# Kernel tuning notes

Measured on AMD Instinct MI355X. Metric: run time of the kernel, lower is better.

## Reference

```python
import jax, jax.numpy as jnp
import numpy as np

B, S, D, H = 4, 1024, 1024, 16
DH = D // H  # 64
SCALE = 1.0 / np.sqrt(D)  # module uses 1/sqrt(d_model), not d_head


def _mh(t):
    # [B,S,D] -> [B*H,S,DH]
    b, s, _ = t.shape
    return t.reshape(b, s, H, DH).transpose(0, 2, 1, 3).reshape(b * H, s, DH)


def _shift(t):
    # pad one zero at FRONT of last dim, reinterpret (row-major) as [BH,L+1,S], drop first row
    bh, s, l = t.shape
    t = jnp.concatenate([jnp.zeros((bh, s, 1), t.dtype), t], axis=-1)
    return t.reshape(bh, l + 1, s)[:, 1:, :]


def setup_inputs() -> dict:
    key = jax.random.key(0)
    ks = jax.random.split(key, 12)
    w_sc = 1.0 / np.sqrt(D)
    return {
        "x": jax.random.normal(ks[0], (B, S, D), jnp.float32),
        "u": jax.random.normal(ks[1], (DH,), jnp.float32) * 0.02,
        "v": jax.random.normal(ks[2], (DH,), jnp.float32) * 0.02,
        "pos": jax.random.normal(ks[3], (B, S, D), jnp.float32),
        "Wq": jax.random.normal(ks[4], (D, D), jnp.float32) * w_sc,
        "bq": jnp.zeros((D,), jnp.float32),
        "Wk": jax.random.normal(ks[5], (D, D), jnp.float32) * w_sc,
        "bk": jnp.zeros((D,), jnp.float32),
        "Wv": jax.random.normal(ks[6], (D, D), jnp.float32) * w_sc,
        "bv": jnp.zeros((D,), jnp.float32),
        "Wc": jax.random.normal(ks[7], (D, D), jnp.float32) * w_sc,
        "bc": jnp.zeros((D,), jnp.float32),
    }


def reference(x, u, v, pos, Wq, bq, Wk, bk, Wv, bv, Wc, bc):
    q = _mh(x @ Wq.T + bq)      # [BH,S,DH]
    k = _mh(x @ Wk.T + bk)      # [BH,S,DH]
    w = _mh(x @ Wv.T + bv)      # [BH,S,DH]
    r = _mh(pos)                # [BH,S,DH]
    ac = jnp.einsum('bjk,bmk->bjm', q + u, k)          # content-content  [BH,S,S]
    bd = _shift(jnp.einsum('bjk,blk->bjl', q + v, r))  # content-position [BH,S,S]
    att = jax.nn.softmax((ac + bd) * SCALE, axis=-1)   # dropout is identity (eval)
    o = att @ w                                        # [BH,S,DH]
    o = o.reshape(B, H, S, DH).transpose(0, 2, 1, 3).reshape(B, S, D)
    return o @ Wc.T + bc
```

## Files before the change

### kernel.cpp

```cpp
#include <hip/hip_runtime.h>
#include <hip/hip_bf16.h>


typedef __bf16 bf16x8 __attribute__((ext_vector_type(8)));
typedef float  f32x4  __attribute__((ext_vector_type(4)));
typedef unsigned short u16x4 __attribute__((ext_vector_type(4)));

struct alignas(16) U128 { unsigned long long lo, hi; };

__device__ __forceinline__ bf16x8 ldg8(const __hip_bfloat16* p) {
    U128 u = *reinterpret_cast<const U128*>(p);
    return __builtin_bit_cast(bf16x8, u);
}

__device__ __forceinline__ __bf16 f2b(float f) {
    __hip_bfloat16 h = __float2bfloat16(f);
    return __builtin_bit_cast(__bf16, h);
}
__device__ __forceinline__ unsigned short f2bu(float f) {
    __hip_bfloat16 h = __float2bfloat16(f);
    return __builtin_bit_cast(unsigned short, h);
}
__device__ __forceinline__ float b2f(__bf16 b) {
    __hip_bfloat16 h = __builtin_bit_cast(__hip_bfloat16, b);
    return __bfloat162float(h);
}

__device__ __forceinline__ bf16x8 ldg8cvt(const float* p) {
    f32x4 a = *reinterpret_cast<const f32x4*>(p);
    f32x4 b = *reinterpret_cast<const f32x4*>(p + 4);
    bf16x8 r;
    r[0] = f2b(a[0]); r[1] = f2b(a[1]); r[2] = f2b(a[2]); r[3] = f2b(a[3]);
    r[4] = f2b(b[0]); r[5] = f2b(b[1]); r[6] = f2b(b[2]); r[7] = f2b(b[3]);
    return r;
}

#define MFMA16(a, b, c) __builtin_amdgcn_mfma_f32_16x16x32_bf16((a), (b), (c), 0, 0, 0)

__device__ __forceinline__ void gll16(const __hip_bfloat16* g, void* lds_wave_base) {
    __builtin_amdgcn_global_load_lds(
        (const __attribute__((address_space(1))) void*)g,
        (__attribute__((address_space(3))) void*)lds_wave_base,
        16, 0, 0);
}

__global__ __launch_bounds__(256) void cvt_kernel(
    const float* __restrict__ x,  const float* __restrict__ pos,
    const float* __restrict__ wq, const float* __restrict__ wk,
    const float* __restrict__ wv, const float* __restrict__ wc,
    __hip_bfloat16* __restrict__ xb, __hip_bfloat16* __restrict__ posb,
    __hip_bfloat16* __restrict__ wqkvb, __hip_bfloat16* __restrict__ wcb)
{
    const size_t base = ((size_t)blockIdx.x * 256 + threadIdx.x) * 8;
    const size_t M1 = (size_t)1 << 20;
    const float* src; __hip_bfloat16* dst; size_t o;
    if (base < 4*M1)        { src = x;   dst = xb;           o = base; }
    else if (base < 8*M1)   { src = pos; dst = posb;         o = base - 4*M1; }
    else if (base < 9*M1)   { src = wq;  dst = wqkvb;        o = base - 8*M1; }
    else if (base < 10*M1)  { src = wk;  dst = wqkvb + M1;   o = base - 9*M1; }
    else if (base < 11*M1)  { src = wv;  dst = wqkvb + 2*M1; o = base - 10*M1; }
    else                    { src = wc;  dst = wcb;          o = base - 11*M1; }
    *(bf16x8*)(dst + o) = ldg8cvt(src + o);
}

__global__ __launch_bounds__(256) void gemm_qkv(
    const __hip_bfloat16* __restrict__ A,
    const __hip_bfloat16* __restrict__ Bm,
    const float* __restrict__ bq, const float* __restrict__ bk,
    const float* __restrict__ bv, const float* __restrict__ u,
    __hip_bfloat16* __restrict__ Qu,
    __hip_bfloat16* __restrict__ Kb, __hip_bfloat16* __restrict__ Vt)
{
    __shared__ __hip_bfloat16 As[128 * 32];
    __shared__ __hip_bfloat16 Bs[128 * 32];

    const int tid  = threadIdx.x;
    const int lane = tid & 63, w = tid >> 6;
    const int quad = lane >> 4, c16 = lane & 15;
    const int wm = w >> 1, wn = w & 1;
    const int m0 = blockIdx.y * 128;
    const int n0 = blockIdx.x * 128;

    const int srow = w * 16 + (lane >> 2);
    const int scol = (lane & 3) * 8;
    const __hip_bfloat16* gA0 = A  + (size_t)(m0 + srow) * 1024 + scol;
    const __hip_bfloat16* gA1 = gA0 + (size_t)64 * 1024;
    const __hip_bfloat16* gB0 = Bm + (size_t)(n0 + srow) * 1024 + scol;
    const __hip_bfloat16* gB1 = gB0 + (size_t)64 * 1024;
    char* ldsA0 = (char*)As + (w << 10);
    char* ldsA1 = ldsA0 + 4096;
    char* ldsB0 = (char*)Bs + (w << 10);
    char* ldsB1 = ldsB0 + 4096;

    f32x4 acc[4][4] = {};

    for (int k0 = 0; k0 < 1024; k0 += 32) {
        gll16(gA0 + k0, ldsA0);
        gll16(gA1 + k0, ldsA1);
        gll16(gB0 + k0, ldsB0);
        gll16(gB1 + k0, ldsB1);
        __syncthreads();

        bf16x8 af[4], bfr[4];
        #pragma unroll
        for (int i = 0; i < 4; ++i) {
            af[i]  = *(const bf16x8*)&As[(wm * 64 + i * 16 + c16) * 32 + quad * 8];
            bfr[i] = *(const bf16x8*)&Bs[(wn * 64 + i * 16 + c16) * 32 + quad * 8];
        }
        #pragma unroll
        for (int mi = 0; mi < 4; ++mi)
            #pragma unroll
            for (int ni = 0; ni < 4; ++ni)
                acc[mi][ni] = MFMA16(af[mi], bfr[ni], acc[mi][ni]);
        __syncthreads();
    }

    #pragma unroll
    for (int mi = 0; mi < 4; ++mi) {
        #pragma unroll
        for (int ni = 0; ni < 4; ++ni) {
            const int m = m0 + wm * 64 + mi * 16 + quad * 4;
            const int n = n0 + wn * 64 + ni * 16 + c16;
            if (n < 1024) {
                const float b0 = bq[n] + u[n & 63];
                #pragma unroll
                for (int r = 0; r < 4; ++r)
                    Qu[(size_t)(m + r) * 1024 + n] =
                        __float2bfloat16(acc[mi][ni][r] + b0);
            } else if (n < 2048) {
                const int nn = n - 1024;
                const float b0 = bk[nn];
                #pragma unroll
                for (int r = 0; r < 4; ++r)
                    Kb[(size_t)(m + r) * 1024 + nn] =
                        __float2bfloat16(acc[mi][ni][r] + b0);
            } else {
                const int nn = n - 2048;
                const float b0 = bv[nn];
                const int d = nn & 63, hh = nn >> 6;
                const int bb = m >> 10, s = m & 1023;
                u16x4 pk;
                #pragma unroll
                for (int r = 0; r < 4; ++r)
                    pk[r] = f2bu(acc[mi][ni][r] + b0);
                *(u16x4*)&Vt[(((size_t)(bb * 16 + hh) * 64 + d) << 10) + s] = pk;
            }
        }
    }
}

__global__ __launch_bounds__(256) void gemm_fin64(
    const __hip_bfloat16* __restrict__ A,
    const __hip_bfloat16* __restrict__ Bm,
    float* __restrict__ dout, const float* __restrict__ bc)
{
    __shared__ __hip_bfloat16 As[64 * 32];
    __shared__ __hip_bfloat16 Bs[64 * 32];

    const int tid  = threadIdx.x;
    const int lane = tid & 63, w = tid >> 6;
    const int quad = lane >> 4, c16 = lane & 15;
    const int wm = w >> 1, wn = w & 1;
    const int m0 = blockIdx.y * 64;
    const int n0 = blockIdx.x * 64;

    const int srow = w * 16 + (lane >> 2);
    const int scol = (lane & 3) * 8;
    const __hip_bfloat16* gA = A  + (size_t)(m0 + srow) * 1024 + scol;
    const __hip_bfloat16* gB = Bm + (size_t)(n0 + srow) * 1024 + scol;
    char* ldsA = (char*)As + (w << 10);
    char* ldsB = (char*)Bs + (w << 10);

    f32x4 acc[2][2] = {};

    for (int k0 = 0; k0 < 1024; k0 += 32) {
        gll16(gA + k0, ldsA);
        gll16(gB + k0, ldsB);
        __syncthreads();

        bf16x8 af[2], bfr[2];
        #pragma unroll
        for (int i = 0; i < 2; ++i) {
            af[i]  = *(const bf16x8*)&As[(wm * 32 + i * 16 + c16) * 32 + quad * 8];
            bfr[i] = *(const bf16x8*)&Bs[(wn * 32 + i * 16 + c16) * 32 + quad * 8];
        }
        #pragma unroll
        for (int mi = 0; mi < 2; ++mi)
            #pragma unroll
            for (int ni = 0; ni < 2; ++ni)
                acc[mi][ni] = MFMA16(af[mi], bfr[ni], acc[mi][ni]);
        __syncthreads();
    }

    #pragma unroll
    for (int mi = 0; mi < 2; ++mi) {
        #pragma unroll
        for (int ni = 0; ni < 2; ++ni) {
            const int m = m0 + wm * 32 + mi * 16 + quad * 4;
            const int n = n0 + wn * 32 + ni * 16 + c16;
            const float b0 = bc[n];
            #pragma unroll
            for (int r = 0; r < 4; ++r)
                dout[(size_t)(m + r) * 1024 + n] = acc[mi][ni][r] + b0;
        }
    }
}

__device__ __forceinline__ int lidx16(int row, int c) {
    return (row << 10) + ((((c >> 3) ^ row) << 3) | (c & 7));
}

__global__ __launch_bounds__(512) void attn_kernel(
    const __hip_bfloat16* __restrict__ Qu,
    const __hip_bfloat16* __restrict__ Kb,
    const __hip_bfloat16* __restrict__ Posb,
    const __hip_bfloat16* __restrict__ Vt,
    const float* __restrict__ uvec, const float* __restrict__ vvec,
    __hip_bfloat16* __restrict__ O)
{
    __shared__ __hip_bfloat16 Ls[64 * 1024];
    __shared__ float q2s[64];
    __shared__ float Wsum[64 * 8];
    __shared__ float rs[64];

    const int tid  = threadIdx.x;
    const int lane = tid & 63, w = tid >> 6;
    const int quad = lane >> 4, c16 = lane & 15;
    const int i0 = blockIdx.x * 64;
    const int bh = blockIdx.y;
    const int b = bh >> 4, h = bh & 15;
    const size_t headoff = (size_t)h * 64;
    const size_t tokbase = (size_t)b * 1024;
    const int j2 = i0 + 64;

    if (tid < 64) {
        float val = 0.f;
        if (j2 < 1024)
            val = b2f(__builtin_bit_cast(__bf16,
                      Qu[(tokbase + j2) * 1024 + headoff + tid])) +
                  (vvec[tid] - uvec[tid]);
        q2s[tid] = val;
    }
    __syncthreads();

    if (tid < 64) {
        const int i = i0 + tid;
        if (i + 1 < 1024) Ls[lidx16(tid, i + 1)] = __float2bfloat16(0.f);
    }

    const __hip_bfloat16* qup0 =
        Qu + (tokbase + i0 + c16) * 1024 + headoff + quad * 8;

    {
        bf16x8 a[4][2];
        #pragma unroll
        for (int g = 0; g < 4; ++g) {
            a[g][0] = ldg8(qup0 + (size_t)g * 16 * 1024);
            a[g][1] = ldg8(qup0 + (size_t)g * 16 * 1024 + 32);
            #pragma unroll
            for (int j = 0; j < 8; ++j) {
                const int d = quad * 8 + j;
                a[g][0][j] = f2b(b2f(a[g][0][j]) + (vvec[d] - uvec[d]));
                a[g][1][j] = f2b(b2f(a[g][1][j]) + (vvec[d + 32] - uvec[d + 32]));
            }
        }
        for (int t = 0; t < 8; ++t) {
            const int l0 = w * 128 + t * 16;
            const __hip_bfloat16* rp =
                Posb + (tokbase + l0 + c16) * 1024 + headoff + quad * 8;
            const bf16x8 r0 = ldg8(rp);
            const bf16x8 r1 = ldg8(rp + 32);
            const int l = l0 + c16;
            #pragma unroll
            for (int g = 0; g < 4; ++g) {
                f32x4 c = (f32x4){0.f, 0.f, 0.f, 0.f};
                c = MFMA16(a[g][0], r0, c);
                c = MFMA16(a[g][1], r1, c);
                #pragma unroll
                for (int r = 0; r < 4; ++r) {
                    const int jl = g * 16 + quad * 4 + r;
                    const int j  = i0 + jl;
                    const __bf16 val = f2b(c[r]);
                    if (l >= 1023 - j) Ls[lidx16(jl, l + j - 1023)] =
                        __builtin_bit_cast(__hip_bfloat16, val);
                    if (jl >= 1 && l <= 1022 - j) Ls[lidx16(jl - 1, l + j + 1)] =
                        __builtin_bit_cast(__hip_bfloat16, val);
                }
            }
        }
    }

    if (j2 < 1024) {
        for (int c = i0 + 65 + tid; c < 1024; c += 512) {
            const int l = c - i0 - 65;
            const __hip_bfloat16* rp = Posb + (tokbase + l) * 1024 + headoff;
            float s = 0.f;
            #pragma unroll
            for (int d8 = 0; d8 < 8; ++d8) {
                const bf16x8 rv = ldg8(rp + d8 * 8);
                #pragma unroll
                for (int j = 0; j < 8; ++j)
                    s += q2s[d8 * 8 + j] * b2f(rv[j]);
            }
            Ls[lidx16(63, c)] = __float2bfloat16(s);
        }
    }
    __syncthreads();

    {
        bf16x8 au[4][2];
        #pragma unroll
        for (int g = 0; g < 4; ++g) {
            au[g][0] = ldg8(qup0 + (size_t)g * 16 * 1024);
            au[g][1] = ldg8(qup0 + (size_t)g * 16 * 1024 + 32);
        }
        const float C1 = 1.44269504f * 0.03125f;
        const float C2 = -5.77078016f;
        float sums[4][4] = {};
        for (int t = 0; t < 8; ++t) {
            const int c0 = w * 128 + t * 16;
            const __hip_bfloat16* kp =
                Kb + (tokbase + c0 + c16) * 1024 + headoff + quad * 8;
            const bf16x8 k0 = ldg8(kp);
            const bf16x8 k1 = ldg8(kp + 32);
            const int cc = c0 + c16;
            #pragma unroll
            for (int g = 0; g < 4; ++g) {
                f32x4 c = (f32x4){0.f, 0.f, 0.f, 0.f};
                c = MFMA16(au[g][0], k0, c);
                c = MFMA16(au[g][1], k1, c);
                #pragma unroll
                for (int r = 0; r < 4; ++r) {
                    const int il = g * 16 + quad * 4 + r;
                    const int idx = lidx16(il, cc);
                    const float lg = __bfloat162float(Ls[idx]) + c[r];
                    const float p = __builtin_amdgcn_exp2f(fmaf(lg, C1, C2));
                    sums[g][r] += p;
                    Ls[idx] = __float2bfloat16(p);
                }
            }
        }
        #pragma unroll
        for (int g = 0; g < 4; ++g)
            #pragma unroll
            for (int r = 0; r < 4; ++r) {
                float s = sums[g][r];
                s += __shfl_xor(s, 1);
                s += __shfl_xor(s, 2);
                s += __shfl_xor(s, 4);
                s += __shfl_xor(s, 8);
                if (c16 == 0) Wsum[(g * 16 + quad * 4 + r) * 8 + w] = s;
            }
    }
    __syncthreads();

    if (tid < 64) {
        float s = 0.f;
        #pragma unroll
        for (int k = 0; k < 8; ++k) s += Wsum[tid * 8 + k];
        rs[tid] = 1.f / s;
    }
    __syncthreads();

    {
        const int d0 = (w & 3) * 16;
        const int kh = w >> 2;
        const __hip_bfloat16* vp =
            Vt + ((size_t)bh * 64 + d0 + c16) * 1024 + quad * 8;
        f32x4 acc[4] = {};
        for (int kk = kh * 512; kk < kh * 512 + 512; kk += 32) {
            const bf16x8 vld = ldg8(vp + kk);
            #pragma unroll
            for (int g = 0; g < 4; ++g) {
                const bf16x8 p =
                    *(const bf16x8*)&Ls[lidx16(g * 16 + c16, kk + quad * 8)];
                acc[g] = MFMA16(p, vld, acc[g]);
            }
        }
        __syncthreads();
        float* Lf = (float*)Ls;
        const int sbase = (w & 3) * 1024;
        if (kh == 1) {
            #pragma unroll
            for (int g = 0; g < 4; ++g)
                #pragma unroll
                for (int r = 0; r < 4; ++r)
                    Lf[sbase + g * 256 + (quad * 4 + r) * 16 + c16] = acc[g][r];
        }
        __syncthreads();
        if (kh == 0) {
            #pragma unroll
            for (int g = 0; g < 4; ++g)
                #pragma unroll
                for (int r = 0; r < 4; ++r) {
                    const int il = g * 16 + quad * 4 + r;
                    const float val =
                        (acc[g][r] + Lf[sbase + g * 256 + (quad * 4 + r) * 16 + c16])
                        * rs[il];
                    const int i = i0 + il;
                    const int d = d0 + c16;
                    O[(tokbase + i) * 1024 + headoff + d] = __float2bfloat16(val);
                }
        }
    }
}

extern "C" void kernel_launch(void* const* d_in, const int* in_sizes, int n_in,
                              void* d_out, int out_size, void* d_ws, size_t ws_size,
                              hipStream_t stream)
{
    const float* x   = (const float*)d_in[0];
    const float* u   = (const float*)d_in[1];
    const float* v   = (const float*)d_in[2];
    const float* pos = (const float*)d_in[3];
    const float* Wq  = (const float*)d_in[4];
    const float* bq  = (const float*)d_in[5];
    const float* Wk  = (const float*)d_in[6];
    const float* bk  = (const float*)d_in[7];
    const float* Wv  = (const float*)d_in[8];
    const float* bv  = (const float*)d_in[9];
    const float* Wc  = (const float*)d_in[10];
    const float* bc  = (const float*)d_in[11];

    const size_t MB = (size_t)1 << 20;
    char* ws = (char*)d_ws;
    __hip_bfloat16* Qu    = (__hip_bfloat16*)(ws + 0 * MB);
    __hip_bfloat16* Kb    = (__hip_bfloat16*)(ws + 8 * MB);
    __hip_bfloat16* Vt    = (__hip_bfloat16*)(ws + 16 * MB);
    __hip_bfloat16* xb    = (__hip_bfloat16*)(ws + 24 * MB);
    __hip_bfloat16* O     = (__hip_bfloat16*)(ws + 24 * MB);
    __hip_bfloat16* Posb  = (__hip_bfloat16*)(ws + 32 * MB);
    __hip_bfloat16* Wqkvb = (__hip_bfloat16*)(ws + 40 * MB);
    __hip_bfloat16* Wcb   = (__hip_bfloat16*)(ws + 46 * MB);

    cvt_kernel<<<6144, 256, 0, stream>>>(x, pos, Wq, Wk, Wv, Wc,
                                         xb, Posb, Wqkvb, Wcb);

    gemm_qkv<<<dim3(24, 32), dim3(256), 0, stream>>>(
        xb, Wqkvb, bq, bk, bv, u, Qu, Kb, Vt);

    attn_kernel<<<dim3(16, 64), dim3(512), 0, stream>>>(
        Qu, Kb, Posb, Vt, u, v, O);

    gemm_fin64<<<dim3(16, 64), dim3(256), 0, stream>>>(
        O, Wcb, (float*)d_out, bc);
}
```

Before: 287.3 us.

## Double attention block threads to 1024 and enlarge output GEMM M-tile to 128

The attention kernel now runs 16 waves per block instead of 8. Each wave covers half as many positions and keys, and the P·V reduction is split four ways with a three-way partial sum through LDS. Separately, the output projection GEMM uses 128-row tiles with four M-fragments per wave, which halves the grid and raises reuse of each B tile. The extra waves aim to hide latency in the LDS-bound attention block, at the cost of more register pressure under the 1024-thread launch bound and more cross-wave reduction traffic.

```diff
diff --git a/kernel.cpp b/kernel.cpp
--- a/kernel.cpp
+++ b/kernel.cpp
@@ -149,43 +149,47 @@
     }
 }
 
-__global__ __launch_bounds__(256) void gemm_fin64(
+__global__ __launch_bounds__(256) void gemm_fin(
     const __hip_bfloat16* __restrict__ A,
     const __hip_bfloat16* __restrict__ Bm,
     float* __restrict__ dout, const float* __restrict__ bc)
 {
-    __shared__ __hip_bfloat16 As[64 * 32];
+    __shared__ __hip_bfloat16 As[128 * 32];
     __shared__ __hip_bfloat16 Bs[64 * 32];
 
     const int tid  = threadIdx.x;
     const int lane = tid & 63, w = tid >> 6;
     const int quad = lane >> 4, c16 = lane & 15;
     const int wm = w >> 1, wn = w & 1;
-    const int m0 = blockIdx.y * 64;
+    const int m0 = blockIdx.y * 128;
     const int n0 = blockIdx.x * 64;
 
     const int srow = w * 16 + (lane >> 2);
     const int scol = (lane & 3) * 8;
-    const __hip_bfloat16* gA = A  + (size_t)(m0 + srow) * 1024 + scol;
-    const __hip_bfloat16* gB = Bm + (size_t)(n0 + srow) * 1024 + scol;
-    char* ldsA = (char*)As + (w << 10);
-    char* ldsB = (char*)Bs + (w << 10);
-
-    f32x4 acc[2][2] = {};
+    const __hip_bfloat16* gA0 = A  + (size_t)(m0 + srow) * 1024 + scol;
+    const __hip_bfloat16* gA1 = gA0 + (size_t)64 * 1024;
+    const __hip_bfloat16* gB0 = Bm + (size_t)(n0 + srow) * 1024 + scol;
+    char* ldsA0 = (char*)As + (w << 10);
+    char* ldsA1 = ldsA0 + 4096;
+    char* ldsB0 = (char*)Bs + (w << 10);
+
+    f32x4 acc[4][2] = {};
 
     for (int k0 = 0; k0 < 1024; k0 += 32) {
-        gll16(gA + k0, ldsA);
-        gll16(gB + k0, ldsB);
-        __syncthreads();
-
-        bf16x8 af[2], bfr[2];
-        #pragma unroll
-        for (int i = 0; i < 2; ++i) {
-            af[i]  = *(const bf16x8*)&As[(wm * 32 + i * 16 + c16) * 32 + quad * 8];
+        gll16(gA0 + k0, ldsA0);
+        gll16(gA1 + k0, ldsA1);
+        gll16(gB0 + k0, ldsB0);
+        __syncthreads();
+
+        bf16x8 af[4], bfr[2];
+        #pragma unroll
+        for (int i = 0; i < 4; ++i)
+            af[i] = *(const bf16x8*)&As[(wm * 64 + i * 16 + c16) * 32 + quad * 8];
+        #pragma unroll
+        for (int i = 0; i < 2; ++i)
             bfr[i] = *(const bf16x8*)&Bs[(wn * 32 + i * 16 + c16) * 32 + quad * 8];
-        }
-        #pragma unroll
-        for (int mi = 0; mi < 2; ++mi)
+        #pragma unroll
+        for (int mi = 0; mi < 4; ++mi)
             #pragma unroll
             for (int ni = 0; ni < 2; ++ni)
                 acc[mi][ni] = MFMA16(af[mi], bfr[ni], acc[mi][ni]);
@@ -193,10 +197,10 @@
     }
 
     #pragma unroll
-    for (int mi = 0; mi < 2; ++mi) {
+    for (int mi = 0; mi < 4; ++mi) {
         #pragma unroll
         for (int ni = 0; ni < 2; ++ni) {
-            const int m = m0 + wm * 32 + mi * 16 + quad * 4;
+            const int m = m0 + wm * 64 + mi * 16 + quad * 4;
             const int n = n0 + wn * 32 + ni * 16 + c16;
             const float b0 = bc[n];
             #pragma unroll
@@ -210,7 +214,7 @@
     return (row << 10) + ((((c >> 3) ^ row) << 3) | (c & 7));
 }
 
-__global__ __launch_bounds__(512) void attn_kernel(
+__global__ __launch_bounds__(1024) void attn_kernel(
     const __hip_bfloat16* __restrict__ Qu,
     const __hip_bfloat16* __restrict__ Kb,
     const __hip_bfloat16* __restrict__ Posb,
@@ -220,7 +224,7 @@
 {
     __shared__ __hip_bfloat16 Ls[64 * 1024];
     __shared__ float q2s[64];
-    __shared__ float Wsum[64 * 8];
+    __shared__ float Wsum[64 * 16];
     __shared__ float rs[64];
 
     const int tid  = threadIdx.x;
@@ -264,8 +268,8 @@
                 a[g][1][j] = f2b(b2f(a[g][1][j]) + (vvec[d + 32] - uvec[d + 32]));
             }
         }
-        for (int t = 0; t < 8; ++t) {
-            const int l0 = w * 128 + t * 16;
+        for (int t = 0; t < 4; ++t) {
+            const int l0 = w * 64 + t * 16;
             const __hip_bfloat16* rp =
                 Posb + (tokbase + l0 + c16) * 1024 + headoff + quad * 8;
             const bf16x8 r0 = ldg8(rp);
@@ -291,7 +295,7 @@
     }
 
     if (j2 < 1024) {
-        for (int c = i0 + 65 + tid; c < 1024; c += 512) {
+        for (int c = i0 + 65 + tid; c < 1024; c += 1024) {
             const int l = c - i0 - 65;
             const __hip_bfloat16* rp = Posb + (tokbase + l) * 1024 + headoff;
             float s = 0.f;
@@ -317,8 +321,8 @@
         const float C1 = 1.44269504f * 0.03125f;
         const float C2 = -5.77078016f;
         float sums[4][4] = {};
-        for (int t = 0; t < 8; ++t) {
-            const int c0 = w * 128 + t * 16;
+        for (int t = 0; t < 4; ++t) {
+            const int c0 = w * 64 + t * 16;
             const __hip_bfloat16* kp =
                 Kb + (tokbase + c0 + c16) * 1024 + headoff + quad * 8;
             const bf16x8 k0 = ldg8(kp);
@@ -349,7 +353,7 @@
                 s += __shfl_xor(s, 2);
                 s += __shfl_xor(s, 4);
                 s += __shfl_xor(s, 8);
-                if (c16 == 0) Wsum[(g * 16 + quad * 4 + r) * 8 + w] = s;
+                if (c16 == 0) Wsum[(g * 16 + quad * 4 + r) * 16 + w] = s;
             }
     }
     __syncthreads();
@@ -357,7 +361,7 @@
     if (tid < 64) {
         float s = 0.f;
         #pragma unroll
-        for (int k = 0; k < 8; ++k) s += Wsum[tid * 8 + k];
+        for (int k = 0; k < 16; ++k) s += Wsum[tid * 16 + k];
         rs[tid] = 1.f / s;
     }
     __syncthreads();
@@ -368,7 +372,7 @@
         const __hip_bfloat16* vp =
             Vt + ((size_t)bh * 64 + d0 + c16) * 1024 + quad * 8;
         f32x4 acc[4] = {};
-        for (int kk = kh * 512; kk < kh * 512 + 512; kk += 32) {
+        for (int kk = kh * 256; kk < kh * 256 + 256; kk += 32) {
             const bf16x8 vld = ldg8(vp + kk);
             #pragma unroll
             for (int g = 0; g < 4; ++g) {
@@ -379,8 +383,8 @@
         }
         __syncthreads();
         float* Lf = (float*)Ls;
-        const int sbase = (w & 3) * 1024;
-        if (kh == 1) {
+        if (kh != 0) {
+            const int sbase = ((kh - 1) * 4 + (w & 3)) * 1024;
             #pragma unroll
             for (int g = 0; g < 4; ++g)
                 #pragma unroll
@@ -394,9 +398,12 @@
                 #pragma unroll
                 for (int r = 0; r < 4; ++r) {
                     const int il = g * 16 + quad * 4 + r;
-                    const float val =
-                        (acc[g][r] + Lf[sbase + g * 256 + (quad * 4 + r) * 16 + c16])
-                        * rs[il];
+                    float val = acc[g][r];
+                    #pragma unroll
+                    for (int q = 1; q < 4; ++q)
+                        val += Lf[((q - 1) * 4 + (w & 3)) * 1024 + g * 256 +
+                                  (quad * 4 + r) * 16 + c16];
+                    val *= rs[il];
                     const int i = i0 + il;
                     const int d = d0 + c16;
                     O[(tokbase + i) * 1024 + headoff + d] = __float2bfloat16(val);
@@ -439,9 +446,9 @@
     gemm_qkv<<<dim3(24, 32), dim3(256), 0, stream>>>(
         xb, Wqkvb, bq, bk, bv, u, Qu, Kb, Vt);
 
-    attn_kernel<<<dim3(16, 64), dim3(512), 0, stream>>>(
+    attn_kernel<<<dim3(16, 64), dim3(1024), 0, stream>>>(
         Qu, Kb, Posb, Vt, u, v, O);
 
-    gemm_fin64<<<dim3(16, 64), dim3(256), 0, stream>>>(
+    gemm_fin<<<dim3(16, 32), dim3(256), 0, stream>>>(
         O, Wcb, (float*)d_out, bc);
 }
```

Measured after the change: 318.3 us. 10.8% more time.
